# Performance work log

Measured on AMD Instinct MI355X. Metric: run time of the kernel, lower is better.

## Reference

```python
import jax, jax.numpy as jnp
import numpy as np

K = 3       # attractive nearest neighbors
J = 3       # repulsive offset (uses dist[:, :, J:])
ALPHA = 0.1
NU = 1e-3


def setup_inputs() -> dict:
    key = jax.random.key(0)
    k1, k2 = jax.random.split(key, 2)
    phi_p = jax.random.normal(k1, (4, 512, 64, 64), dtype=jnp.float32)
    memory_bank = jax.random.normal(k2, (16384, 512), dtype=jnp.float32)
    r = jnp.ones((1,), dtype=jnp.float32)
    return {"phi_p": phi_p, "memory_bank": memory_bank, "r": r}


def reference(phi_p, memory_bank, r):
    B, C, H, W = phi_p.shape
    # b c h w -> b (h w) c
    x = phi_p.reshape(B, C, H * W).transpose(0, 2, 1)
    x2 = jnp.sum(x * x, axis=-1, keepdims=True)            # [B, HW, 1]
    m2 = jnp.sum(memory_bank * memory_bank, axis=-1)       # [N]
    d2 = x2 + m2[None, None, :] - 2.0 * jnp.einsum('bnc,mc->bnm', x, memory_bank)
    d2 = jnp.maximum(d2, 0.0)                              # [B, HW, N]
    # smallest K+J squared distances, ascending (topk(largest=False))
    neg_top, _ = jax.lax.top_k(-d2, K + J)
    dist = -neg_top                                        # [B, HW, K+J]
    r2 = r ** 2
    scores_att = dist[:, :, :K] - r2
    loss_att = jnp.mean(jnp.maximum(scores_att, 0.0)) / NU
    scores_rep = r2 - dist[:, :, J:] - ALPHA
    loss_rep = jnp.mean(jnp.maximum(scores_rep, 0.0)) / NU
    return loss_att + loss_rep
```

## Files before the change

kernel.cpp:

```cpp
#include <hip/hip_runtime.h>
#include <cfloat>

#define B_   4
#define C_   512
#define HW_  4096
#define R_   16384
#define N_   16384
#define ALPHA_ 0.1f
#define SCALE_ ((float)(1000.0/49152.0))

typedef unsigned int u32;
typedef unsigned short u16;
typedef unsigned char u8;
typedef __attribute__((ext_vector_type(2))) unsigned long long u64x2;
typedef __attribute__((ext_vector_type(4))) float f32x4;
typedef __attribute__((ext_vector_type(16))) float f32x16;

typedef const __attribute__((address_space(1))) u32* gas_u32;
typedef __attribute__((address_space(3))) u32* las_u32;

__device__ __forceinline__ void async16(const void* g, void* l) {
    __builtin_amdgcn_global_load_lds((gas_u32)g, (las_u32)l, 16, 0, 0);
}

__device__ __forceinline__ u32 pk_fp8x4(float a, float b, float c, float d) {
    u32 v = __builtin_amdgcn_cvt_pk_fp8_f32(a, b, 0, false);
    v = __builtin_amdgcn_cvt_pk_fp8_f32(c, d, v, true);
    return v;
}

__device__ __forceinline__ void ins6(float (&t)[6], float v) {
    if (v < t[5]) {
        t[5] = v;
        #pragma unroll
        for (int q = 5; q >= 1; --q) {
            float lo = fminf(t[q-1], t[q]);
            float hi = fmaxf(t[q-1], t[q]);
            t[q-1] = lo; t[q] = hi;
        }
    }
}


__global__ void conv_mem_kernel(const float* __restrict__ mem,
                                u8* __restrict__ Mb, float* __restrict__ m2) {
    int w = threadIdx.x >> 6, l = threadIdx.x & 63;
    int row = blockIdx.x * 4 + w;
    const float4* p = (const float4*)(mem + (size_t)row * C_);
    float4 a = p[l], b = p[l + 64];
    float s = a.x*a.x + a.y*a.y + a.z*a.z + a.w*a.w
            + b.x*b.x + b.y*b.y + b.z*b.z + b.w*b.w;
    u8* base = Mb + (size_t)(row >> 5) * 16384;
    int r31 = row & 31;
    {
        int kb = 4 * l;
        *(u32*)(base + ((kb>>4)>>1)*1024 + ((((kb>>3)&1)<<5) + r31)*16
                + ((kb>>4)&1)*8 + (kb&4)) = pk_fp8x4(a.x, a.y, a.z, a.w);
    }
    {
        int kb = 256 + 4 * l;
        *(u32*)(base + ((kb>>4)>>1)*1024 + ((((kb>>3)&1)<<5) + r31)*16
                + ((kb>>4)&1)*8 + (kb&4)) = pk_fp8x4(b.x, b.y, b.z, b.w);
    }
    #pragma unroll
    for (int off = 32; off > 0; off >>= 1) s += __shfl_down(s, off);
    if (l == 0) m2[row] = s;
}

__global__ void conv_phi_kernel(const float* __restrict__ phi, u8* __restrict__ Xb,
                                float* __restrict__ x2) {
    __shared__ float T[64][65];
    int t = threadIdx.x;
    int n0 = blockIdx.x * 64, c0 = blockIdx.y * 64, b = blockIdx.z;
    const float* src = phi + ((size_t)b * C_ + c0) * HW_ + n0;
    int l = t & 63, cg = t >> 6;
    float sq = 0.f;
    #pragma unroll
    for (int p = 0; p < 16; ++p) {
        int c = cg + p * 4;
        float v = src[(size_t)c * HW_ + l];
        T[c][l] = v;
        sq = fmaf(v, v, sq);
    }
    atomicAdd(&x2[(size_t)b * HW_ + n0 + l], sq);
    __syncthreads();
    int cq = t & 15, gl0 = t >> 4;
    #pragma unroll
    for (int p = 0; p < 4; ++p) {
        int gl = gl0 + p * 16;
        u32 v = pk_fp8x4(T[cq*4+0][gl], T[cq*4+1][gl],
                         T[cq*4+2][gl], T[cq*4+3][gl]);
        int g = (int)((size_t)b * HW_ + n0 + gl);
        int kb = c0 + cq * 4;
        *(u32*)(Xb + (size_t)(g >> 5) * 16384 + ((kb>>4)>>1)*1024
                + ((((kb>>3)&1)<<5) + (g & 31))*16 + ((kb>>4)&1)*8 + (kb&4)) = v;
    }
}

template<int NC>
__global__ __launch_bounds__(256, 3) void gemm_topk_kernel(
    const u8* __restrict__ Xb, const u8* __restrict__ Mb,
    const float* __restrict__ m2, float* __restrict__ P ) {
    __shared__ __align__(16) u8 smem[16384];
    const int t = threadIdx.x;
    const int w = t >> 6, l = t & 63;
    const int id   = blockIdx.x;
    const int xcd  = id & 7;
    const int cy   = (xcd * NC) >> 3;
    const int xsub = xcd - cy * (8 / NC);
    const int bx   = (id >> 3) + xsub * (128 * NC / 8);
    const int g0   = bx * 128;
    const int n0c  = cy * (N_ / NC);
    const int n32c = n0c >> 5;
    const int xt   = (g0 >> 5) + w;
    const int col  = l & 31, h = l >> 5;

    float top[6];
    #pragma unroll
    for (int q = 0; q < 6; ++q) top[q] = FLT_MAX;

    {
        const u8* Msrc = Mb + (size_t)(n32c + w) * 16384;
        #pragma unroll
        for (int pp = 0; pp < 2; ++pp)
            async16(Msrc + pp*1024 + l*16, smem + w*2048 + pp*1024);
    }
    __syncthreads();

    const int NT = N_ / NC / 128;
    #pragma unroll 1
    for (int nt = 0; nt < NT; ++nt) {
        f32x16 acc[4];
        #pragma unroll
        for (int n = 0; n < 4; ++n) acc[n] = (f32x16)0.f;

        #pragma unroll
        for (int s = 0; s < 8; ++s) {
            const int cur = (nt * 8 + s) & 1;
            u64x2 xv0 = *(const u64x2*)(Xb + ((size_t)xt*16 + 2*s  )*1024 + l*16);
            u64x2 xv1 = *(const u64x2*)(Xb + ((size_t)xt*16 + 2*s+1)*1024 + l*16);
            {
                const int gs2 = nt * 8 + s + 1;
                if (gs2 < NT * 8) {
                    const int nt2 = gs2 >> 3, s2 = gs2 & 7;
                    const u8* Msrc = Mb + (size_t)(n32c + nt2*4 + w) * 16384
                                        + (size_t)(2*s2) * 1024;
                    u8* dst = smem + (cur^1)*8192 + w*2048;
                    #pragma unroll
                    for (int pp = 0; pp < 2; ++pp)
                        async16(Msrc + pp*1024 + l*16, dst + pp*1024);
                }
            }
            const u8* buf = smem + cur*8192;
            #pragma unroll
            for (int pp = 0; pp < 2; ++pp) {
                const u64x2 xv = pp ? xv1 : xv0;
                #pragma unroll
                for (int tt = 0; tt < 4; ++tt) {
                    u64x2 bm = *(const u64x2*)(buf + tt*2048 + pp*1024 + l*16);
                    acc[tt] = __builtin_amdgcn_mfma_f32_32x32x16_fp8_fp8(
                        (long)bm.x, (long)xv.x, acc[tt], 0, 0, 0);
                    acc[tt] = __builtin_amdgcn_mfma_f32_32x32x16_fp8_fp8(
                        (long)bm.y, (long)xv.y, acc[tt], 0, 0, 0);
                }
            }

            if (s == 7) {
                const int n0 = n0c + nt * 128;
                #pragma unroll
                for (int tt = 0; tt < 4; ++tt) {
                    const f32x4* m2p = (const f32x4*)(m2 + n0 + tt*32 + h*4);
                    float dv[16];
                    float vmin = FLT_MAX;
                    #pragma unroll
                    for (int gq = 0; gq < 4; ++gq) {
                        f32x4 mv = m2p[gq * 2];
                        #pragma unroll
                        for (int c = 0; c < 4; ++c) {
                            float d = mv[c] - 2.f * acc[tt][gq*4 + c];
                            dv[gq*4 + c] = d;
                            vmin = fminf(vmin, d);
                        }
                    }
                    if (vmin < top[5]) {
                        #pragma unroll
                        for (int i = 0; i < 16; ++i) ins6(top, dv[i]);
                    }
                }
            }
            __syncthreads();
        }
    }

    float* Mg = (float*)smem;
    {
        int lrow = w * 32 + col;
        #pragma unroll
        for (int q = 0; q < 6; ++q)
            Mg[lrow * 13 + h * 6 + q] = top[q];
    }
    __syncthreads();
    if (t < 128) {
        float t6[6];
        #pragma unroll
        for (int q = 0; q < 6; ++q) t6[q] = FLT_MAX;
        const float* row = Mg + t * 13;
        #pragma unroll
        for (int v = 0; v < 12; ++v) ins6(t6, row[v]);
        float* dst = P + ((size_t)(g0 + t) * NC + cy) * 6;
        #pragma unroll
        for (int q = 0; q < 6; ++q) dst[q] = t6[q];
    }
}

template<int NC>
__global__ void finalize_kernel(const float* __restrict__ P, const float* __restrict__ x2,
                                const float* __restrict__ rp, float* __restrict__ out) {
    int g = blockIdx.x * 256 + threadIdx.x;
    float t6[6];
    #pragma unroll
    for (int q = 0; q < 6; ++q) t6[q] = FLT_MAX;
    const f32x4* pp = (const f32x4*)(P + (size_t)g * (NC * 6));
    #pragma unroll
    for (int q = 0; q < NC * 6 / 4; ++q) {
        f32x4 v = pp[q];
        ins6(t6, v.x); ins6(t6, v.y); ins6(t6, v.z); ins6(t6, v.w);
    }
    float x2g = x2[g];
    float rv = rp[0], r2 = rv * rv;
    float s = 0.f;
    #pragma unroll
    for (int i = 0; i < 3; ++i) {
        float d = fmaxf(t6[i] + x2g, 0.f);
        s += fmaxf(d - r2, 0.f);
    }
    #pragma unroll
    for (int i = 3; i < 6; ++i) {
        float d = fmaxf(t6[i] + x2g, 0.f);
        s += fmaxf(r2 - d - ALPHA_, 0.f);
    }
    #pragma unroll
    for (int off = 32; off > 0; off >>= 1) s += __shfl_down(s, off);
    __shared__ float red[4];
    int w = threadIdx.x >> 6, l = threadIdx.x & 63;
    if (l == 0) red[w] = s;
    __syncthreads();
    if (threadIdx.x == 0)
        atomicAdd(out, (red[0] + red[1] + red[2] + red[3]) * SCALE_);
}

#define TM 64
#define TN 64
#define KC 64
#define LDP 68

__global__ void m2_kernel(const float* __restrict__ mem, float* __restrict__ m2) {
    int wave = threadIdx.x >> 6, lane = threadIdx.x & 63;
    int row = blockIdx.x * 4 + wave;
    const float4* p = reinterpret_cast<const float4*>(mem + (size_t)row * C_);
    float4 a = p[lane], b = p[lane + 64];
    float s = a.x*a.x + a.y*a.y + a.z*a.z + a.w*a.w
            + b.x*b.x + b.y*b.y + b.z*b.z + b.w*b.w;
    #pragma unroll
    for (int off = 32; off > 0; off >>= 1) s += __shfl_down(s, off);
    if (lane == 0) m2[row] = s;
}

__global__ void x2f_kernel(const float* __restrict__ phi, float* __restrict__ x2) {
    int g = blockIdx.x * blockDim.x + threadIdx.x;
    int b = g >> 12;
    int n = g & 4095;
    const float* p = phi + (size_t)b * C_ * HW_ + n;
    float s = 0.f;
    #pragma unroll 8
    for (int c = 0; c < C_; ++c) {
        float v = p[(size_t)c * HW_];
        s = fmaf(v, v, s);
    }
    x2[g] = s;
}

__global__ __launch_bounds__(256) void dist_loss_kernel(
    const float* __restrict__ phi, const float* __restrict__ mem,
    const float* __restrict__ rp,  const float* __restrict__ m2,
    const float* __restrict__ x2,  float* __restrict__ out) {
    __shared__ float smem[2 * TM * LDP];
    float* xs = smem;
    float* ms = smem + TM * LDP;
    const int tid = threadIdx.x;
    const int tx = tid & 15, ty = tid >> 4;
    const int g0 = blockIdx.x * TM;
    const int b = g0 >> 12, n0img = g0 & 4095;
    const float* phiB = phi + (size_t)b * C_ * HW_ + n0img;
    float top[4][6];
    #pragma unroll
    for (int i = 0; i < 4; ++i)
        #pragma unroll
        for (int q = 0; q < 6; ++q) top[i][q] = FLT_MAX;
    float x2v[4];
    #pragma unroll
    for (int i = 0; i < 4; ++i) x2v[i] = x2[g0 + ty * 4 + i];
    for (int nt = 0; nt < N_ / TN; ++nt) {
        const int n0 = nt * TN;
        float acc[4][4];
        #pragma unroll
        for (int i = 0; i < 4; ++i)
            #pragma unroll
            for (int j = 0; j < 4; ++j) acc[i][j] = 0.f;
        for (int s = 0; s < C_ / KC; ++s) {
            const int k0 = s * KC;
            {
                int rr = tid & 63, cb = tid >> 6;
                #pragma unroll
                for (int p = 0; p < 16; ++p) {
                    int cc = p * 4 + cb;
                    xs[rr * LDP + cc] = phiB[(size_t)(k0 + cc) * HW_ + rr];
                }
            }
            {
                int kq = tid & 15, cb = tid >> 4;
                #pragma unroll
                for (int p = 0; p < 4; ++p) {
                    int c = p * 16 + cb;
                    float4 v = *reinterpret_cast<const float4*>(
                        mem + (size_t)(n0 + c) * C_ + k0 + kq * 4);
                    ms[(kq*4+0)*LDP + c] = v.x; ms[(kq*4+1)*LDP + c] = v.y;
                    ms[(kq*4+2)*LDP + c] = v.z; ms[(kq*4+3)*LDP + c] = v.w;
                }
            }
            __syncthreads();
            #pragma unroll
            for (int kq = 0; kq < KC / 4; ++kq) {
                float4 xa[4], mb[4];
                #pragma unroll
                for (int i = 0; i < 4; ++i)
                    xa[i] = *reinterpret_cast<const float4*>(&xs[(ty*4+i)*LDP + kq*4]);
                #pragma unroll
                for (int kk = 0; kk < 4; ++kk)
                    mb[kk] = *reinterpret_cast<const float4*>(&ms[(kq*4+kk)*LDP + tx*4]);
                #pragma unroll
                for (int i = 0; i < 4; ++i) {
                    const float xk[4] = {xa[i].x, xa[i].y, xa[i].z, xa[i].w};
                    #pragma unroll
                    for (int kk = 0; kk < 4; ++kk) {
                        const float mc[4] = {mb[kk].x, mb[kk].y, mb[kk].z, mb[kk].w};
                        #pragma unroll
                        for (int j = 0; j < 4; ++j)
                            acc[i][j] = fmaf(xk[kk], mc[j], acc[i][j]);
                    }
                }
            }
            __syncthreads();
        }
        #pragma unroll
        for (int j = 0; j < 4; ++j) {
            float m2v = m2[n0 + tx * 4 + j];
            #pragma unroll
            for (int i = 0; i < 4; ++i) {
                float d = fmaxf(x2v[i] + m2v - 2.f * acc[i][j], 0.f);
                ins6(top[i], d);
            }
        }
    }
    __syncthreads();
    float* mg = smem;
    #pragma unroll
    for (int i = 0; i < 4; ++i)
        #pragma unroll
        for (int q = 0; q < 6; ++q)
            mg[(ty*4+i)*97 + tx*6 + q] = top[i][q];
    __syncthreads();
    if (tid < 64) {
        float t6[6];
        #pragma unroll
        for (int q = 0; q < 6; ++q) t6[q] = FLT_MAX;
        const float* row = mg + tid * 97;
        for (int v = 0; v < 96; ++v) ins6(t6, row[v]);
        float rv = rp[0], r2 = rv * rv;
        float s = fmaxf(t6[0]-r2,0.f) + fmaxf(t6[1]-r2,0.f) + fmaxf(t6[2]-r2,0.f)
                + fmaxf(r2-t6[3]-ALPHA_,0.f) + fmaxf(r2-t6[4]-ALPHA_,0.f)
                + fmaxf(r2-t6[5]-ALPHA_,0.f);
        #pragma unroll
        for (int off = 32; off > 0; off >>= 1) s += __shfl_down(s, off);
        if (tid == 0) atomicAdd(out, s * SCALE_);
    }
}

extern "C" void kernel_launch(void* const* d_in, const int* in_sizes, int n_in,
                              void* d_out, int out_size, void* d_ws, size_t ws_size,
                              hipStream_t stream) {
    const float* phi = (const float*)d_in[0];
    const float* mem = (const float*)d_in[1];
    const float* rp  = (const float*)d_in[2];
    float* out = (float*)d_out;

    const size_t offX  = 0;
    const size_t offM  = (size_t)R_ * C_;
    const size_t offx2 = offM + (size_t)N_ * C_;
    const size_t offm2 = offx2 + (size_t)R_ * 4;
    const size_t offP  = offm2 + (size_t)N_ * 4;
    const size_t need8 = offP + (size_t)R_ * 8 * 6 * 4;
    const size_t need4 = offP + (size_t)R_ * 4 * 6 * 4;

    hipMemsetAsync(out, 0, sizeof(float), stream);

    if (ws_size >= need4) {
        u8*    Xb = (u8*)((char*)d_ws + offX);
        u8*    Mb = (u8*)((char*)d_ws + offM);
        float* x2 = (float*)((char*)d_ws + offx2);
        float* m2 = (float*)((char*)d_ws + offm2);
        float* P  = (float*)((char*)d_ws + offP);

        hipMemsetAsync(x2, 0, (size_t)R_ * 4, stream);
        conv_mem_kernel<<<N_ / 4, 256, 0, stream>>>(mem, Mb, m2);
        conv_phi_kernel<<<dim3(HW_ / 64, C_ / 64, B_), 256, 0, stream>>>(phi, Xb, x2);
        if (ws_size >= need8) {
            gemm_topk_kernel<8><<<dim3(128 * 8, 1), 256, 0, stream>>>(Xb, Mb, m2, P);
            finalize_kernel<8><<<R_ / 256, 256, 0, stream>>>(P, x2, rp, out);
        } else {
            gemm_topk_kernel<4><<<dim3(128 * 4, 1), 256, 0, stream>>>(Xb, Mb, m2, P);
            finalize_kernel<4><<<R_ / 256, 256, 0, stream>>>(P, x2, rp, out);
        }
    } else {
        float* m2 = (float*)d_ws;
        float* x2 = m2 + N_;
        m2_kernel<<<N_ / 4, 256, 0, stream>>>(mem, m2);
        x2f_kernel<<<R_ / 256, 256, 0, stream>>>(phi, x2);
        dist_loss_kernel<<<R_ / TM, 256, 0, stream>>>(phi, mem, rp, m2, x2, out);
    }
}
```

Baseline: 342.4 us.

## Double rows per warp in fp8 GEMM-topk to reuse memory-bank LDS tiles

Each warp now computes two 32-row tiles of query rows instead of one, so each LDS-loaded memory-bank fragment feeds twice as many MFMAs. Block tile grows from 128 to 256 rows and the grid is halved. The intent is to cut LDS reads, global M reloads per row and sync overhead per FLOP. The cost is double the accumulators (128 acc VGPRs), which is why launch bounds drop to 2 blocks per CU, and a grid of 512 blocks may underfill 256 CUs.

```diff
diff --git a/kernel.cpp b/kernel.cpp
--- a/kernel.cpp
+++ b/kernel.cpp
@@ -98,7 +98,7 @@
 }
 
 template<int NC>
-__global__ __launch_bounds__(256, 3) void gemm_topk_kernel(
+__global__ __launch_bounds__(256, 2) void gemm_topk_kernel(
     const u8* __restrict__ Xb, const u8* __restrict__ Mb,
     const float* __restrict__ m2, float* __restrict__ P ) {
     __shared__ __align__(16) u8 smem[16384];
@@ -108,16 +108,18 @@
     const int xcd  = id & 7;
     const int cy   = (xcd * NC) >> 3;
     const int xsub = xcd - cy * (8 / NC);
-    const int bx   = (id >> 3) + xsub * (128 * NC / 8);
-    const int g0   = bx * 128;
+    const int bx   = (id >> 3) + xsub * (64 * NC / 8);
+    const int g0   = bx * 256;
     const int n0c  = cy * (N_ / NC);
     const int n32c = n0c >> 5;
-    const int xt   = (g0 >> 5) + w;
+    const int xt0  = (g0 >> 5) + w * 2;
     const int col  = l & 31, h = l >> 5;
 
-    float top[6];
-    #pragma unroll
-    for (int q = 0; q < 6; ++q) top[q] = FLT_MAX;
+    float top[2][6];
+    #pragma unroll
+    for (int u = 0; u < 2; ++u)
+        #pragma unroll
+        for (int q = 0; q < 6; ++q) top[u][q] = FLT_MAX;
 
     {
         const u8* Msrc = Mb + (size_t)(n32c + w) * 16384;
@@ -130,15 +132,22 @@
     const int NT = N_ / NC / 128;
     #pragma unroll 1
     for (int nt = 0; nt < NT; ++nt) {
-        f32x16 acc[4];
-        #pragma unroll
-        for (int n = 0; n < 4; ++n) acc[n] = (f32x16)0.f;
+        f32x16 acc[2][4];
+        #pragma unroll
+        for (int u = 0; u < 2; ++u)
+            #pragma unroll
+            for (int n = 0; n < 4; ++n) acc[u][n] = (f32x16)0.f;
 
         #pragma unroll
         for (int s = 0; s < 8; ++s) {
             const int cur = (nt * 8 + s) & 1;
-            u64x2 xv0 = *(const u64x2*)(Xb + ((size_t)xt*16 + 2*s  )*1024 + l*16);
-            u64x2 xv1 = *(const u64x2*)(Xb + ((size_t)xt*16 + 2*s+1)*1024 + l*16);
+            u64x2 xv[2][2];
+            #pragma unroll
+            for (int u = 0; u < 2; ++u)
+                #pragma unroll
+                for (int pp = 0; pp < 2; ++pp)
+                    xv[u][pp] = *(const u64x2*)(
+                        Xb + ((size_t)(xt0 + u)*16 + 2*s + pp)*1024 + l*16);
             {
                 const int gs2 = nt * 8 + s + 1;
                 if (gs2 < NT * 8) {
@@ -154,53 +163,58 @@
             const u8* buf = smem + cur*8192;
             #pragma unroll
             for (int pp = 0; pp < 2; ++pp) {
-                const u64x2 xv = pp ? xv1 : xv0;
                 #pragma unroll
                 for (int tt = 0; tt < 4; ++tt) {
                     u64x2 bm = *(const u64x2*)(buf + tt*2048 + pp*1024 + l*16);
-                    acc[tt] = __builtin_amdgcn_mfma_f32_32x32x16_fp8_fp8(
-                        (long)bm.x, (long)xv.x, acc[tt], 0, 0, 0);
-                    acc[tt] = __builtin_amdgcn_mfma_f32_32x32x16_fp8_fp8(
-                        (long)bm.y, (long)xv.y, acc[tt], 0, 0, 0);
+                    #pragma unroll
+                    for (int u = 0; u < 2; ++u) {
+                        acc[u][tt] = __builtin_amdgcn_mfma_f32_32x32x16_fp8_fp8(
+                            (long)bm.x, (long)xv[u][pp].x, acc[u][tt], 0, 0, 0);
+                        acc[u][tt] = __builtin_amdgcn_mfma_f32_32x32x16_fp8_fp8(
+                            (long)bm.y, (long)xv[u][pp].y, acc[u][tt], 0, 0, 0);
+                    }
                 }
             }
 
             if (s == 7) {
                 const int n0 = n0c + nt * 128;
                 #pragma unroll
-                for (int tt = 0; tt < 4; ++tt) {
-                    const f32x4* m2p = (const f32x4*)(m2 + n0 + tt*32 + h*4);
-                    float dv[16];
-                    float vmin = FLT_MAX;
+                for (int u = 0; u < 2; ++u)
                     #pragma unroll
-                    for (int gq = 0; gq < 4; ++gq) {
-                        f32x4 mv = m2p[gq * 2];
+                    for (int tt = 0; tt < 4; ++tt) {
+                        const f32x4* m2p = (const f32x4*)(m2 + n0 + tt*32 + h*4);
+                        float dv[16];
+                        float vmin = FLT_MAX;
                         #pragma unroll
-                        for (int c = 0; c < 4; ++c) {
-                            float d = mv[c] - 2.f * acc[tt][gq*4 + c];
-                            dv[gq*4 + c] = d;
-                            vmin = fminf(vmin, d);
+                        for (int gq = 0; gq < 4; ++gq) {
+                            f32x4 mv = m2p[gq * 2];
+                            #pragma unroll
+                            for (int c = 0; c < 4; ++c) {
+                                float d = mv[c] - 2.f * acc[u][tt][gq*4 + c];
+                                dv[gq*4 + c] = d;
+                                vmin = fminf(vmin, d);
+                            }
+                        }
+                        if (vmin < top[u][5]) {
+                            #pragma unroll
+                            for (int i = 0; i < 16; ++i) ins6(top[u], dv[i]);
                         }
                     }
-                    if (vmin < top[5]) {
-                        #pragma unroll
-                        for (int i = 0; i < 16; ++i) ins6(top, dv[i]);
-                    }
-                }
             }
             __syncthreads();
         }
     }
 
     float* Mg = (float*)smem;
+    #pragma unroll
+    for (int u = 0; u < 2; ++u) {
+        int lrow = w * 64 + u * 32 + col;
+        #pragma unroll
+        for (int q = 0; q < 6; ++q)
+            Mg[lrow * 13 + h * 6 + q] = top[u][q];
+    }
+    __syncthreads();
     {
-        int lrow = w * 32 + col;
-        #pragma unroll
-        for (int q = 0; q < 6; ++q)
-            Mg[lrow * 13 + h * 6 + q] = top[q];
-    }
-    __syncthreads();
-    if (t < 128) {
         float t6[6];
         #pragma unroll
         for (int q = 0; q < 6; ++q) t6[q] = FLT_MAX;
@@ -415,10 +429,10 @@
         conv_mem_kernel<<<N_ / 4, 256, 0, stream>>>(mem, Mb, m2);
         conv_phi_kernel<<<dim3(HW_ / 64, C_ / 64, B_), 256, 0, stream>>>(phi, Xb, x2);
         if (ws_size >= need8) {
-            gemm_topk_kernel<8><<<dim3(128 * 8, 1), 256, 0, stream>>>(Xb, Mb, m2, P);
+            gemm_topk_kernel<8><<<dim3(64 * 8, 1), 256, 0, stream>>>(Xb, Mb, m2, P);
             finalize_kernel<8><<<R_ / 256, 256, 0, stream>>>(P, x2, rp, out);
         } else {
-            gemm_topk_kernel<4><<<dim3(128 * 4, 1), 256, 0, stream>>>(Xb, Mb, m2, P);
+            gemm_topk_kernel<4><<<dim3(64 * 4, 1), 256, 0, stream>>>(Xb, Mb, m2, P);
             finalize_kernel<4><<<R_ / 256, 256, 0, stream>>>(P, x2, rp, out);
         }
     } else {
```

New measurement: 344.8 us. No clear change (+0.7%).
